# Performance work log

Hardware: AMD Instinct MI355X
Metric: run time of the kernel (lower is better)

The kernel has to match this reference:

```python
import jax, jax.numpy as jnp
import numpy as np

T = 4096          # timesteps per modality
D_QK = 64
D = D_QK + 2      # feature dim incl. timestamp channel = 66
M = 4             # number of modalities
N_LIN = 3         # n_layers=2 hidden layers -> 3 Linear layers in the MLP


def setup_inputs() -> dict:
    key = jax.random.key(0)
    ks = jax.random.split(key, 2 * M + 2)
    inp = {}
    for m in range(M):
        feats = jax.random.normal(ks[2 * m], (1, 1, T, D - 1), dtype=jnp.float32)
        # last feature channel is a sorted event timestamp, as the source reads X[0,0,:,-1]
        ts = jnp.sort(jax.random.uniform(ks[2 * m + 1], (T,), dtype=jnp.float32))
        inp[f"x{m + 1}"] = jnp.concatenate([feats, ts[None, None, :, None]], axis=-1)
    scale = 1.0 / np.sqrt(D).astype(np.float32)
    inp["wq"] = jax.random.normal(ks[2 * M], (N_LIN, D, D), dtype=jnp.float32) * scale
    inp["bq"] = jnp.zeros((N_LIN, D), dtype=jnp.float32)
    inp["wk"] = jax.random.normal(ks[2 * M + 1], (N_LIN, D, D), dtype=jnp.float32) * scale
    inp["bk"] = jnp.zeros((N_LIN, D), dtype=jnp.float32)
    return inp


def _mlp(x, W, b):
    # MLP(d, [d]*2, d, relu): relu after hidden linears, none after the last
    h = x
    for i in range(N_LIN - 1):
        h = jax.nn.relu(h @ W[i] + b[i])
    return h @ W[N_LIN - 1] + b[N_LIN - 1]


def _causal_dot_product(Q, K, V, t1, t2):
    """Cross-modality causal linear attention with timestamps.
    Q:(T1,d) queries at times t1; K:(T2,d), V:(T2,dv) at times t2 (sorted).
    out[i] = Q[i] @ sum_{j : t2[j] <= t1[i]} K[j] (x) V[j]
    Implemented as a cumulative outer-product state + gather (scan form).
    """
    state = jnp.cumsum(K[:, :, None] * V[:, None, :], axis=0)   # (T2, d, dv)
    idx = jnp.searchsorted(t2, t1, side="right") - 1            # last key with t2 <= t1[i]
    S = state[jnp.clip(idx, 0)]                                  # (T1, d, dv)
    S = jnp.where((idx >= 0)[:, None, None], S, jnp.zeros_like(S))
    return jnp.einsum("td,tdv->tv", Q, S)                        # (T1, dv)


def reference(x1, x2, x3, x4, wq, bq, wk, bk):
    xs = [x1, x2, x3, x4]
    Q = _mlp(x1, wq, bq)[0, 0]      # (T1, D)
    t1 = x1[0, 0, :, -1]
    outs = []
    for xm in xs:                   # fixed small loop over M modalities
        Km = _mlp(xm, wk, bk)[0, 0]  # shared W_K[0], as in the source
        Vm = xm[0, 0]                # V = X
        t2 = xm[0, 0, :, -1]
        outs.append(_causal_dot_product(Q, Km, Vm, t1, t2))
    Z = jnp.stack(outs, axis=0)     # (M, T1, D) == Zout[0]
    yhat = Z.sum(0)[None, :, :2]    # (1, T1, 2)
    return yhat
```

## Files before the change

### kernel.cpp

```cpp
#include <hip/hip_runtime.h>

#define T 4096
#define D 66
#define NL 3
#define NC 64
#define JC 64
#define HS 68
#define WS 68
#define DD (D * D)

__global__ __launch_bounds__(256) void mlp_scan_kernel(
    const float* __restrict__ x1, const float* __restrict__ x2,
    const float* __restrict__ x3, const float* __restrict__ x4,
    const float* __restrict__ wq, const float* __restrict__ bq,
    const float* __restrict__ wk, const float* __restrict__ bk,
    float* __restrict__ Q, float* __restrict__ S,
    float* __restrict__ chunkSum, float* __restrict__ TM)
{
    __shared__ float ht[2][D * HS];
    __shared__ float Wl[D * WS];
    const int t    = threadIdx.x;
    const bool isQ = blockIdx.x >= 256;
    const int m    = isQ ? 0 : (blockIdx.x >> 6);
    const int j0   = (isQ ? (blockIdx.x - 256) : (blockIdx.x & 63)) * 64;
    const float* X = (isQ || m == 0) ? x1 : (m == 1 ? x2 : (m == 2 ? x3 : x4));
    const float* W = isQ ? wq : wk;
    const float* Bs = isQ ? bq : bk;

    const float* xt = X + (size_t)j0 * D;
#pragma unroll 4
    for (int k = t; k < 64 * D; k += 256) {
        const int r = k / D;
        const int d = k - r * D;
        ht[0][d * HS + r] = xt[k];
    }

    float wreg[18];
#pragma unroll
    for (int i = 0; i < 18; ++i) {
        const int k = t + i * 256;
        if (k < DD) wreg[i] = W[k];
    }

    const int lane = t & 63;
    const int wv   = t >> 6;
    const int og   = lane & 15;
    const int rg   = lane >> 4;
    const int r0   = wv * 16 + rg * 4;
    const int c0   = og * 4;

    int src = 0;
#pragma unroll 1
    for (int l = 0; l < NL; ++l) {
#pragma unroll
        for (int i = 0; i < 18; ++i) {
            const int k = t + i * 256;
            if (k < DD) {
                const int d = k / D;
                const int o = k - d * D;
                Wl[d * WS + o] = wreg[i];
            }
        }
        __syncthreads();

        if (l < NL - 1) {
            const float* Wg = W + (l + 1) * DD;
#pragma unroll
            for (int i = 0; i < 18; ++i) {
                const int k = t + i * 256;
                if (k < DD) wreg[i] = Wg[k];
            }
        }

        float acc[4][4];
        float acce[4];
        {
            const float b0 = Bs[l * D + c0 + 0];
            const float b1 = Bs[l * D + c0 + 1];
            const float b2 = Bs[l * D + c0 + 2];
            const float b3 = Bs[l * D + c0 + 3];
            const float be = Bs[l * D + 64 + (og & 1)];
#pragma unroll
            for (int ri = 0; ri < 4; ++ri) {
                acc[ri][0] = b0; acc[ri][1] = b1;
                acc[ri][2] = b2; acc[ri][3] = b3;
                acce[ri] = be;
            }
        }

        const float* hs = ht[src];
#pragma unroll 6
        for (int d = 0; d < D; ++d) {
            const float4 h4 = *(const float4*)&hs[d * HS + r0];
            const float4 w4 = *(const float4*)&Wl[d * WS + c0];
            const float we  = Wl[d * WS + 64 + (og & 1)];
            const float hv[4] = {h4.x, h4.y, h4.z, h4.w};
#pragma unroll
            for (int ri = 0; ri < 4; ++ri) {
                acc[ri][0] = fmaf(hv[ri], w4.x, acc[ri][0]);
                acc[ri][1] = fmaf(hv[ri], w4.y, acc[ri][1]);
                acc[ri][2] = fmaf(hv[ri], w4.z, acc[ri][2]);
                acc[ri][3] = fmaf(hv[ri], w4.w, acc[ri][3]);
                acce[ri]   = fmaf(hv[ri], we,  acce[ri]);
            }
        }

        if (l < NL - 1 || !isQ) {
            const bool rel = (l < NL - 1);
            const int nb = 1 - src;
            float* hn = ht[nb];
#pragma unroll
            for (int ri = 0; ri < 4; ++ri) {
#pragma unroll
                for (int ci = 0; ci < 4; ++ci) {
                    const float v = acc[ri][ci];
                    hn[(c0 + ci) * HS + r0 + ri] = rel ? fmaxf(v, 0.0f) : v;
                }
                if (og < 2) {
                    const float v = acce[ri];
                    hn[(64 + og) * HS + r0 + ri] = rel ? fmaxf(v, 0.0f) : v;
                }
            }
            __syncthreads();
            src = nb;
        } else {
#pragma unroll
            for (int ri = 0; ri < 4; ++ri) {
                const int row = j0 + r0 + ri;
                float* rp = Q + (size_t)row * D + c0;
                *(float2*)rp       = make_float2(acc[ri][0], acc[ri][1]);
                *((float2*)rp + 1) = make_float2(acc[ri][2], acc[ri][3]);
                if (og < 2) Q[(size_t)row * D + 64 + og] = acce[ri];
            }
        }
    }

    if (!isQ) {
        const int c = t;
        if (c >= 144 && c < 144 + JC) {
            const int j = j0 + (c - 144);
            TM[m * T + j] = X[(size_t)j * D + (D - 1)];
        }
        if (c < 132) {
            const int d = c >> 1;
            const int v = c & 1;
            const float* kcol = &ht[src][d * HS];
            float run = 0.0f;
#pragma unroll 8
            for (int jj = 0; jj < JC; ++jj) {
                run = fmaf(kcol[jj], X[(size_t)(j0 + jj) * D + v], run);
                S[((size_t)m * T + j0 + jj) * 132 + c] = run;
            }
            chunkSum[((size_t)m * NC + (j0 >> 6)) * 132 + c] = run;
        }
    }
}

__global__ __launch_bounds__(256) void chunkscan_kernel(
    const float* __restrict__ chunkSum, float* __restrict__ chunkOff)
{
    const int wv   = threadIdx.x >> 6;
    const int lane = threadIdx.x & 63;
    const int c    = blockIdx.x * 4 + wv;
    const int m    = blockIdx.y;
    if (c >= 132) return;

    const float v = chunkSum[((size_t)m * NC + lane) * 132 + c];
    float inc = v;
#pragma unroll
    for (int off = 1; off < 64; off <<= 1) {
        const float y = __shfl_up(inc, off);
        if (lane >= off) inc += y;
    }
    chunkOff[((size_t)m * NC + lane) * 132 + c] = inc - v;
}

__global__ __launch_bounds__(256) void out_kernel(
    const float* __restrict__ Q, const float* __restrict__ S,
    const float* __restrict__ chunkOff, const float* __restrict__ TM,
    float* __restrict__ out)
{
    __shared__ float segEnd[4][64];
    const int w    = threadIdx.x >> 6;
    const int lane = threadIdx.x & 63;
    const int i    = blockIdx.x * 4 + w;

    segEnd[w][lane] = TM[w * T + lane * 64 + 63];
    const float t1i = TM[i];
    const float q0  = Q[(size_t)i * D + lane];
    const float q1  = (lane < 2) ? Q[(size_t)i * D + 64 + lane] : 0.0f;
    float acc0 = 0.0f, acc1 = 0.0f;
    __syncthreads();

    int seg[4];
#pragma unroll
    for (int m = 0; m < 4; ++m) {
        const unsigned long long b = __ballot(segEnd[m][lane] <= t1i);
        const int hi = __popcll(b);
        seg[m] = (hi < 63) ? hi : 63;
    }
    int idx[4];
#pragma unroll
    for (int m = 0; m < 4; ++m) {
        const float sv = TM[m * T + seg[m] * 64 + lane];
        const unsigned long long b = __ballot(sv <= t1i);
        idx[m] = seg[m] * 64 + __popcll(b) - 1;
    }

#pragma unroll
    for (int m = 0; m < 4; ++m) {
        if (idx[m] >= 0) {
            const float* sp = S + ((size_t)m * T + idx[m]) * 132;
            const float* op = chunkOff + ((size_t)m * NC + (idx[m] / JC)) * 132;
            const float2 s0 = *(const float2*)(sp + lane * 2);
            const float2 c0 = *(const float2*)(op + lane * 2);
            acc0 = fmaf(q0, s0.x + c0.x, acc0);
            acc1 = fmaf(q0, s0.y + c0.y, acc1);
            if (lane < 2) {
                const float2 s1 = *(const float2*)(sp + 128 + lane * 2);
                const float2 c1 = *(const float2*)(op + 128 + lane * 2);
                acc0 = fmaf(q1, s1.x + c1.x, acc0);
                acc1 = fmaf(q1, s1.y + c1.y, acc1);
            }
        }
    }

#pragma unroll
    for (int off = 32; off >= 1; off >>= 1) {
        acc0 += __shfl_down(acc0, off);
        acc1 += __shfl_down(acc1, off);
    }
    if (lane == 0) {
        out[(size_t)i * 2 + 0] = acc0;
        out[(size_t)i * 2 + 1] = acc1;
    }
}

extern "C" void kernel_launch(void* const* d_in, const int* in_sizes, int n_in,
                              void* d_out, int out_size, void* d_ws, size_t ws_size,
                              hipStream_t stream)
{
    (void)in_sizes; (void)n_in; (void)out_size; (void)ws_size;
    const float* x1 = (const float*)d_in[0];
    const float* x2 = (const float*)d_in[1];
    const float* x3 = (const float*)d_in[2];
    const float* x4 = (const float*)d_in[3];
    const float* wq = (const float*)d_in[4];
    const float* bq = (const float*)d_in[5];
    const float* wk = (const float*)d_in[6];
    const float* bk = (const float*)d_in[7];

    float* ws = (float*)d_ws;
    float* Q        = ws;
    float* S        = ws + 270336;
    float* chunkSum = ws + 2433024;
    float* chunkOff = ws + 2466816;
    float* TM       = ws + 2500608;

    mlp_scan_kernel<<<320, 256, 0, stream>>>(x1, x2, x3, x4, wq, bq, wk, bk,
                                             Q, S, chunkSum, TM);
    chunkscan_kernel<<<dim3(33, 4), 256, 0, stream>>>(chunkSum, chunkOff);
    out_kernel<<<1024, 256, 0, stream>>>(Q, S, chunkOff, TM, (float*)d_out);
}
```

Before: 33.75 us.

## Run MLP layers on bf16 MFMA with transposed shared-memory tiles

Replaces the scalar FP32 FMA loop for the three MLP linear layers with bf16 MFMA 16x16x32 instructions. Activations and weights are converted to bf16 and stored row-major and transposed in padded shared memory. The feature dimension is zero-padded to 96 and the output to 80 columns. The V columns and timestamps are cached in shared memory so the scan no longer reloads X from global memory. This cuts ALU time in the MLP, at the cost of bf16 rounding of inputs, weights and hidden activations, which may hurt accuracy.

```diff
diff --git a/kernel.cpp b/kernel.cpp
--- a/kernel.cpp
+++ b/kernel.cpp
@@ -5,9 +5,18 @@
 #define NL 3
 #define NC 64
 #define JC 64
-#define HS 68
-#define WS 68
 #define DD (D * D)
+#define HSB 104
+#define KTS 68
+
+typedef short bf16x8 __attribute__((ext_vector_type(8)));
+typedef float f32x4  __attribute__((ext_vector_type(4)));
+
+__device__ __forceinline__ short f2bf(float f) {
+    unsigned int u = __builtin_bit_cast(unsigned int, f);
+    u += 0x7fff + ((u >> 16) & 1);
+    return (short)(u >> 16);
+}
 
 __global__ __launch_bounds__(256) void mlp_scan_kernel(
     const float* __restrict__ x1, const float* __restrict__ x2,
@@ -17,22 +26,36 @@
     float* __restrict__ Q, float* __restrict__ S,
     float* __restrict__ chunkSum, float* __restrict__ TM)
 {
-    __shared__ float ht[2][D * HS];
-    __shared__ float Wl[D * WS];
+    __shared__ short Hs[64 * HSB];
+    __shared__ short Wt[80 * HSB];
+    __shared__ float KT[D * KTS];
+    __shared__ float side[3][64];
+
     const int t    = threadIdx.x;
     const bool isQ = blockIdx.x >= 256;
     const int m    = isQ ? 0 : (blockIdx.x >> 6);
     const int j0   = (isQ ? (blockIdx.x - 256) : (blockIdx.x & 63)) * 64;
-    const float* X = (isQ || m == 0) ? x1 : (m == 1 ? x2 : (m == 2 ? x3 : x4));
-    const float* W = isQ ? wq : wk;
+    const float* X  = (isQ || m == 0) ? x1 : (m == 1 ? x2 : (m == 2 ? x3 : x4));
+    const float* W  = isQ ? wq : wk;
     const float* Bs = isQ ? bq : bk;
 
     const float* xt = X + (size_t)j0 * D;
-#pragma unroll 4
     for (int k = t; k < 64 * D; k += 256) {
         const int r = k / D;
         const int d = k - r * D;
-        ht[0][d * HS + r] = xt[k];
+        const float v = xt[k];
+        Hs[r * HSB + d] = f2bf(v);
+        if (d < 2) side[d][r] = v;
+        if (d == D - 1) side[2][r] = v;
+    }
+    for (int k = t; k < 64 * (HSB - D); k += 256) {
+        const int r = k / (HSB - D);
+        const int d = D + (k - r * (HSB - D));
+        Hs[r * HSB + d] = 0;
+    }
+    {
+        int* wz = (int*)Wt;
+        for (int k = t; k < 80 * HSB / 2; k += 256) wz[k] = 0;
     }
 
     float wreg[18];
@@ -44,21 +67,21 @@
 
     const int lane = t & 63;
     const int wv   = t >> 6;
-    const int og   = lane & 15;
-    const int rg   = lane >> 4;
-    const int r0   = wv * 16 + rg * 4;
-    const int c0   = og * 4;
-
-    int src = 0;
+    const int lrow = lane & 15;
+    const int kg   = (lane >> 4) * 8;
+    const int cr0  = (lane >> 4) * 4;
+
+    __syncthreads();
+
 #pragma unroll 1
     for (int l = 0; l < NL; ++l) {
 #pragma unroll
         for (int i = 0; i < 18; ++i) {
             const int k = t + i * 256;
             if (k < DD) {
-                const int d = k / D;
-                const int o = k - d * D;
-                Wl[d * WS + o] = wreg[i];
+                const int kk = k / D;
+                const int o  = k - kk * D;
+                Wt[o * HSB + kk] = f2bf(wreg[i]);
             }
         }
         __syncthreads();
@@ -72,86 +95,58 @@
             }
         }
 
-        float acc[4][4];
-        float acce[4];
-        {
-            const float b0 = Bs[l * D + c0 + 0];
-            const float b1 = Bs[l * D + c0 + 1];
-            const float b2 = Bs[l * D + c0 + 2];
-            const float b3 = Bs[l * D + c0 + 3];
-            const float be = Bs[l * D + 64 + (og & 1)];
-#pragma unroll
-            for (int ri = 0; ri < 4; ++ri) {
-                acc[ri][0] = b0; acc[ri][1] = b1;
-                acc[ri][2] = b2; acc[ri][3] = b3;
-                acce[ri] = be;
-            }
-        }
-
-        const float* hs = ht[src];
-#pragma unroll 6
-        for (int d = 0; d < D; ++d) {
-            const float4 h4 = *(const float4*)&hs[d * HS + r0];
-            const float4 w4 = *(const float4*)&Wl[d * WS + c0];
-            const float we  = Wl[d * WS + 64 + (og & 1)];
-            const float hv[4] = {h4.x, h4.y, h4.z, h4.w};
-#pragma unroll
-            for (int ri = 0; ri < 4; ++ri) {
-                acc[ri][0] = fmaf(hv[ri], w4.x, acc[ri][0]);
-                acc[ri][1] = fmaf(hv[ri], w4.y, acc[ri][1]);
-                acc[ri][2] = fmaf(hv[ri], w4.z, acc[ri][2]);
-                acc[ri][3] = fmaf(hv[ri], w4.w, acc[ri][3]);
-                acce[ri]   = fmaf(hv[ri], we,  acce[ri]);
-            }
-        }
-
-        if (l < NL - 1 || !isQ) {
-            const bool rel = (l < NL - 1);
-            const int nb = 1 - src;
-            float* hn = ht[nb];
-#pragma unroll
-            for (int ri = 0; ri < 4; ++ri) {
-#pragma unroll
-                for (int ci = 0; ci < 4; ++ci) {
-                    const float v = acc[ri][ci];
-                    hn[(c0 + ci) * HS + r0 + ri] = rel ? fmaxf(v, 0.0f) : v;
+        const int abase = (wv * 16 + lrow) * HSB + kg;
+        const bf16x8 a0 = *(const bf16x8*)&Hs[abase];
+        const bf16x8 a1 = *(const bf16x8*)&Hs[abase + 32];
+        const bf16x8 a2 = *(const bf16x8*)&Hs[abase + 64];
+
+        f32x4 acc[5];
+#pragma unroll
+        for (int nt = 0; nt < 5; ++nt) {
+            const short* wb = &Wt[(nt * 16 + lrow) * HSB + kg];
+            f32x4 c = {0.0f, 0.0f, 0.0f, 0.0f};
+            c = __builtin_amdgcn_mfma_f32_16x16x32_bf16(a0, *(const bf16x8*)(wb),      c, 0, 0, 0);
+            c = __builtin_amdgcn_mfma_f32_16x16x32_bf16(a1, *(const bf16x8*)(wb + 32), c, 0, 0, 0);
+            c = __builtin_amdgcn_mfma_f32_16x16x32_bf16(a2, *(const bf16x8*)(wb + 64), c, 0, 0, 0);
+            acc[nt] = c;
+        }
+        __syncthreads();
+
+#pragma unroll
+        for (int nt = 0; nt < 5; ++nt) {
+            const int col = nt * 16 + lrow;
+            const float bias = (col < D) ? Bs[l * D + col] : 0.0f;
+#pragma unroll
+            for (int r = 0; r < 4; ++r) {
+                const int row = wv * 16 + cr0 + r;
+                float v = acc[nt][r] + bias;
+                if (l < NL - 1) {
+                    v = fmaxf(v, 0.0f);
+                    Hs[row * HSB + col] = f2bf(v);
+                } else if (isQ) {
+                    if (col < D) Q[(size_t)(j0 + row) * D + col] = v;
+                } else {
+                    if (col < D) KT[col * KTS + row] = v;
                 }
-                if (og < 2) {
-                    const float v = acce[ri];
-                    hn[(64 + og) * HS + r0 + ri] = rel ? fmaxf(v, 0.0f) : v;
-                }
-            }
-            __syncthreads();
-            src = nb;
-        } else {
-#pragma unroll
-            for (int ri = 0; ri < 4; ++ri) {
-                const int row = j0 + r0 + ri;
-                float* rp = Q + (size_t)row * D + c0;
-                *(float2*)rp       = make_float2(acc[ri][0], acc[ri][1]);
-                *((float2*)rp + 1) = make_float2(acc[ri][2], acc[ri][3]);
-                if (og < 2) Q[(size_t)row * D + 64 + og] = acce[ri];
-            }
-        }
-    }
+            }
+        }
+    }
+
+    __syncthreads();
 
     if (!isQ) {
         const int c = t;
-        if (c >= 144 && c < 144 + JC) {
-            const int j = j0 + (c - 144);
-            TM[m * T + j] = X[(size_t)j * D + (D - 1)];
-        }
+        if (c >= 144 && c < 144 + JC) TM[m * T + j0 + (c - 144)] = side[2][c - 144];
         if (c < 132) {
             const int d = c >> 1;
             const int v = c & 1;
-            const float* kcol = &ht[src][d * HS];
             float run = 0.0f;
 #pragma unroll 8
             for (int jj = 0; jj < JC; ++jj) {
-                run = fmaf(kcol[jj], X[(size_t)(j0 + jj) * D + v], run);
+                run = fmaf(KT[d * KTS + jj], side[v][jj], run);
                 S[((size_t)m * T + j0 + jj) * 132 + c] = run;
             }
-            chunkSum[((size_t)m * NC + (j0 >> 6)) * 132 + c] = run;
+            chunkSum[((size_t)m * NC + j0 / JC) * 132 + c] = run;
         }
     }
 }
@@ -194,24 +189,24 @@
 
     int seg[4];
 #pragma unroll
-    for (int m = 0; m < 4; ++m) {
-        const unsigned long long b = __ballot(segEnd[m][lane] <= t1i);
+    for (int mm = 0; mm < 4; ++mm) {
+        const unsigned long long b = __ballot(segEnd[mm][lane] <= t1i);
         const int hi = __popcll(b);
-        seg[m] = (hi < 63) ? hi : 63;
+        seg[mm] = (hi < 63) ? hi : 63;
     }
     int idx[4];
 #pragma unroll
-    for (int m = 0; m < 4; ++m) {
-        const float sv = TM[m * T + seg[m] * 64 + lane];
+    for (int mm = 0; mm < 4; ++mm) {
+        const float sv = TM[mm * T + seg[mm] * 64 + lane];
         const unsigned long long b = __ballot(sv <= t1i);
-        idx[m] = seg[m] * 64 + __popcll(b) - 1;
-    }
-
-#pragma unroll
-    for (int m = 0; m < 4; ++m) {
-        if (idx[m] >= 0) {
-            const float* sp = S + ((size_t)m * T + idx[m]) * 132;
-            const float* op = chunkOff + ((size_t)m * NC + (idx[m] / JC)) * 132;
+        idx[mm] = seg[mm] * 64 + __popcll(b) - 1;
+    }
+
+#pragma unroll
+    for (int mm = 0; mm < 4; ++mm) {
+        if (idx[mm] >= 0) {
+            const float* sp = S + ((size_t)mm * T + idx[mm]) * 132;
+            const float* op = chunkOff + ((size_t)mm * NC + (idx[mm] / JC)) * 132;
             const float2 s0 = *(const float2*)(sp + lane * 2);
             const float2 c0 = *(const float2*)(op + lane * 2);
             acc0 = fmaf(q0, s0.x + c0.x, acc0);
```

New measurement: 29.51 us. -12.6%, faster.
